# Kernel tuning notes

Measured on AMD Instinct MI355X. Metric: run time of the kernel, lower is better.

The kernel has to match this reference:

```python
import jax, jax.numpy as jnp
import numpy as np

N_NODES = 100000
N_EDGES = 1600000
D_FEAT = 64


def setup_inputs() -> dict:
    key = jax.random.key(0)
    k1, k2, k3, k4 = jax.random.split(key, 4)
    input = jax.random.normal(k1, (N_NODES, D_FEAT), dtype=jnp.float32)
    edge_weight = jax.random.uniform(k2, (N_EDGES,), dtype=jnp.float32)
    edge_src = jax.random.randint(k3, (N_EDGES,), 0, N_NODES, dtype=jnp.int64)
    edge_dst = jax.random.randint(k4, (N_EDGES,), 0, N_NODES, dtype=jnp.int64)
    return {"input": input, "edge_weight": edge_weight,
            "edge_src": edge_src, "edge_dst": edge_dst}


def reference(input, edge_weight, edge_src, edge_dst):
    # message: gather source node features, scale by edge weight -> (|E|, d)
    message = input[edge_src] * edge_weight[:, None]
    # aggregate: scatter-add edge messages to destination nodes -> (|V|, d)
    update = jax.ops.segment_sum(message, edge_dst, num_segments=input.shape[0])
    # combine: residual combination of input and update
    return input + update
```

## Files before the change

kernel.cpp:

```cpp
#include <hip/hip_runtime.h>
#include <hip/hip_bf16.h>

#define D_FEAT 64
#define NPB 64
#define NPB_SHIFT 6
#define NL1 128
#define L1_T 512
#define MAX_NB 2048
#define SCAN_T 256
#define SCAN_PER_T 8
#define SCAN_CHUNK (SCAN_T * SCAN_PER_T)
#define SRC_BITS 17
#define SRC_MASK 0x1FFFF
#define CVT_BLOCKS 1024
#define W_SCALE 32768.0f
#define W_INV (1.0f / 32768.0f)
#define SG_T 256
#define MAX_REC 4096

typedef unsigned int uint_t;

__device__ inline unsigned short f32_to_bf16_rn(float f) {
    uint_t x = __float_as_uint(f);
    uint_t r = (x + 0x7fffu + ((x >> 16) & 1u)) >> 16;
    return (unsigned short)r;
}

__global__ void __launch_bounds__(L1_T)
mp_pre_kernel(const int* __restrict__ edst,
              int* __restrict__ counts_T,
              int n_edges, int nb_buckets,
              int* __restrict__ pub) {
    __shared__ int hist[MAX_NB];
    int t = threadIdx.x;
    int b = blockIdx.x;
    if (b == 0)
        for (int i = t; i < 256; i += L1_T) pub[i] = 0;
    for (int k = t; k < nb_buckets; k += L1_T) hist[k] = 0;
    __syncthreads();
    int epb = (n_edges + NL1 - 1) / NL1;
    int lo = b * epb;
    int hi = min(n_edges, lo + epb);
    for (int i = lo + t; i < hi; i += L1_T)
        atomicAdd(&hist[edst[i] >> NPB_SHIFT], 1);
    __syncthreads();
    for (int k = t; k < nb_buckets; k += L1_T)
        counts_T[k * NL1 + b + 1] = hist[k];
    if (b == 0 && t == 0) counts_T[0] = 0;
}

__global__ void mp_scanP_kernel(int* __restrict__ a, int n,
                                int* __restrict__ pub) {
    __shared__ int tsum[SCAN_T];
    __shared__ int red[SCAN_T];
    int t = threadIdx.x, bid = blockIdx.x;
    int base = bid * SCAN_CHUNK + t * SCAN_PER_T;
    int v[SCAN_PER_T];
    int s = 0;
    #pragma unroll
    for (int j = 0; j < SCAN_PER_T; ++j) {
        int idx = base + j;
        v[j] = (idx < n) ? a[idx] : 0;
        s += v[j];
    }
    tsum[t] = s;
    __syncthreads();
    #pragma unroll
    for (int off = 1; off < SCAN_T; off <<= 1) {
        int u = (t >= off) ? tsum[t - off] : 0;
        __syncthreads();
        tsum[t] += u;
        __syncthreads();
    }
    if (t == SCAN_T - 1) atomicExch(&pub[bid], tsum[t] + 1);
    int ls = 0;
    for (int i = t; i < bid; i += SCAN_T) {
        int p;
        while ((p = atomicAdd(&pub[i], 0)) == 0) {}
        ls += p - 1;
    }
    red[t] = ls;
    __syncthreads();
    #pragma unroll
    for (int off = 128; off > 0; off >>= 1) {
        if (t < off) red[t] += red[t + off];
        __syncthreads();
    }
    int run = red[0] + ((t == 0) ? 0 : tsum[t - 1]);
    #pragma unroll
    for (int j = 0; j < SCAN_PER_T; ++j) {
        int idx = base + j;
        run += v[j];
        if (idx < n) a[idx] = run;
    }
}

__global__ void __launch_bounds__(L1_T)
mp_l1scatter_kernel(const int* __restrict__ esrc,
                    const int* __restrict__ edst,
                    const float* __restrict__ ew,
                    const int* __restrict__ counts_T,
                    int2* __restrict__ elistA,
                    int n_edges, int nb_buckets,
                    const float2* __restrict__ in2,
                    uint_t* __restrict__ bfrow, int ncvt) {
    __shared__ int cur[MAX_NB];
    int t = threadIdx.x;
    int b = blockIdx.x;
    if (b < NL1) {
        for (int k = t; k < nb_buckets; k += L1_T)
            cur[k] = counts_T[k * NL1 + b];
        __syncthreads();
        int epb = (n_edges + NL1 - 1) / NL1;
        int lo = b * epb;
        int hi = min(n_edges, lo + epb);
        for (int i = lo + t; i < hi; i += L1_T) {
            int d = edst[i];
            int pos = atomicAdd(&cur[d >> NPB_SHIFT], 1);
            elistA[pos] = make_int2(esrc[i] | ((d & (NPB - 1)) << SRC_BITS),
                                    __float_as_int(ew[i]));
        }
    } else {
        int g0 = (b - NL1) * L1_T + t;
        int stride = CVT_BLOCKS * L1_T;
        for (int g = g0; g < ncvt; g += stride) {
            float2 v = in2[g];
            bfrow[g] = (uint_t)f32_to_bf16_rn(v.x) |
                       ((uint_t)f32_to_bf16_rn(v.y) << 16);
        }
    }
}

__global__ void __launch_bounds__(SG_T)
mp_sortgather_kernel(const float* __restrict__ input,
                     const uint_t* __restrict__ bfrow,
                     const int2* __restrict__ elistA,
                     const int* __restrict__ counts_T,
                     float* __restrict__ out,
                     int n_nodes, int n_edges, int nb_buckets) {
    __shared__ int nh[NPB];
    __shared__ int cur[NPB];
    __shared__ uint_t rec[MAX_REC];
    int k = blockIdx.x;
    int t = threadIdx.x;
    int base = counts_T[k * NL1];
    int end  = (k + 1 < nb_buckets) ? counts_T[(k + 1) * NL1] : n_edges;
    int cnt  = end - base;

    int wv = t >> 6;
    int lane = t & 63;
    int h = lane >> 5, l5 = lane & 31;

    if (cnt <= MAX_REC) {
        if (t < NPB) nh[t] = 0;
        __syncthreads();
        for (int i = t; i < cnt; i += SG_T)
            atomicAdd(&nh[(elistA[base + i].x >> SRC_BITS) & (NPB - 1)], 1);
        __syncthreads();
        #pragma unroll
        for (int off = 1; off < NPB; off <<= 1) {
            int v = (t < NPB && t >= off) ? nh[t - off] : 0;
            __syncthreads();
            if (t < NPB) nh[t] += v;
            __syncthreads();
        }
        if (t < NPB) cur[t] = (t == 0) ? 0 : nh[t - 1];
        __syncthreads();
        for (int i = t; i < cnt; i += SG_T) {
            int2 r = elistA[base + i];
            int node = (r.x >> SRC_BITS) & (NPB - 1);
            int pos = atomicAdd(&cur[node], 1);
            int w15 = (int)(__int_as_float(r.y) * W_SCALE + 0.5f);
            w15 = min(32767, max(0, w15));
            rec[pos] = (uint_t)(r.x & SRC_MASK) | ((uint_t)w15 << 17);
        }
        __syncthreads();

        for (int node = wv; node < NPB; node += (SG_T / 64)) {
            int g = k * NPB + node;
            if (g >= n_nodes) break;
            int sb = (node == 0) ? 0 : nh[node - 1];
            int cn = nh[node] - sb;
            float ax = 0.0f, ay = 0.0f;
            int j = 0;
            for (; j + 16 <= cn; j += 16) {
                uint_t rr[8], u[8];
                #pragma unroll
                for (int q = 0; q < 8; ++q) rr[q] = rec[sb + j + 2 * q + h];
                #pragma unroll
                for (int q = 0; q < 8; ++q)
                    u[q] = bfrow[((rr[q] & SRC_MASK) << 5) + l5];
                #pragma unroll
                for (int q = 0; q < 8; ++q) {
                    float w = (float)(rr[q] >> 17) * W_INV;
                    ax = fmaf(__uint_as_float(u[q] << 16), w, ax);
                    ay = fmaf(__uint_as_float(u[q] & 0xffff0000u), w, ay);
                }
            }
            for (; j < cn; j += 2) {
                int jj = j + h;
                if (jj < cn) {
                    uint_t rr = rec[sb + jj];
                    uint_t u = bfrow[((rr & SRC_MASK) << 5) + l5];
                    float w = (float)(rr >> 17) * W_INV;
                    ax = fmaf(__uint_as_float(u << 16), w, ax);
                    ay = fmaf(__uint_as_float(u & 0xffff0000u), w, ay);
                }
            }
            ax += __shfl_xor(ax, 32, 64);
            ay += __shfl_xor(ay, 32, 64);
            if (h == 0) {
                float2 inp = ((const float2*)input)[((long long)g << 5) + l5];
                float2 o;
                o.x = inp.x + ax;
                o.y = inp.y + ay;
                ((float2*)out)[((long long)g << 5) + l5] = o;
            }
        }
    } else {
        for (int node = wv; node < NPB; node += (SG_T / 64)) {
            int g = k * NPB + node;
            if (g >= n_nodes) break;
            float ax = 0.0f, ay = 0.0f;
            for (int i = h; i < cnt; i += 2) {
                int2 r = elistA[base + i];
                if (((r.x >> SRC_BITS) & (NPB - 1)) == node) {
                    uint_t u = bfrow[(((uint_t)r.x & SRC_MASK) << 5) + l5];
                    float w = __int_as_float(r.y);
                    ax = fmaf(__uint_as_float(u << 16), w, ax);
                    ay = fmaf(__uint_as_float(u & 0xffff0000u), w, ay);
                }
            }
            ax += __shfl_xor(ax, 32, 64);
            ay += __shfl_xor(ay, 32, 64);
            if (h == 0) {
                float2 inp = ((const float2*)input)[((long long)g << 5) + l5];
                float2 o;
                o.x = inp.x + ax;
                o.y = inp.y + ay;
                ((float2*)out)[((long long)g << 5) + l5] = o;
            }
        }
    }
}

__global__ void mp_copy_kernel(const float4* __restrict__ in,
                               float4* __restrict__ out, int n4) {
    int i = blockIdx.x * blockDim.x + threadIdx.x;
    if (i < n4) out[i] = in[i];
}

__global__ void mp_scatter_kernel(const float* __restrict__ input,
                                  const float* __restrict__ ew,
                                  const int* __restrict__ esrc,
                                  const int* __restrict__ edst,
                                  float* __restrict__ out, int n_edges) {
    int tid = blockIdx.x * blockDim.x + threadIdx.x;
    int e = tid >> 6;
    if (e >= n_edges) return;
    int lane = tid & 63;
    float v = input[(long long)esrc[e] * D_FEAT + lane] * ew[e];
    atomicAdd(&out[(long long)edst[e] * D_FEAT + lane], v);
}

extern "C" void kernel_launch(void* const* d_in, const int* in_sizes, int n_in,
                              void* d_out, int out_size, void* d_ws, size_t ws_size,
                              hipStream_t stream) {
    const float* input = (const float*)d_in[0];
    const float* ew    = (const float*)d_in[1];
    const int* esrc    = (const int*)d_in[2];
    const int* edst    = (const int*)d_in[3];
    float* out = (float*)d_out;

    int n_nodes = in_sizes[0] / D_FEAT;
    int n_edges = in_sizes[1];

    int nb_buckets = (n_nodes + NPB - 1) / NPB;
    int n_scan = nb_buckets * NL1 + 1;
    int nbs = (n_scan + SCAN_CHUNK - 1) / SCAN_CHUNK;

    size_t head_ints = (size_t)n_scan + 256;
    size_t elist_off = (head_ints * 4 + 255) & ~(size_t)255;
    size_t elistA_bytes = (size_t)n_edges * 8;
    size_t bf_bytes = (size_t)n_nodes * (D_FEAT * 2);
    size_t needed = elist_off + elistA_bytes + bf_bytes;

    bool ok = (ws_size >= needed) && (nb_buckets <= MAX_NB) &&
              (n_nodes <= (1 << SRC_BITS)) && (nbs <= 256);

    if (ok) {
        int* counts_T = (int*)d_ws;
        int* pub      = counts_T + n_scan;
        int2* elistA  = (int2*)((char*)d_ws + elist_off);
        uint_t* bfrow = (uint_t*)((char*)d_ws + elist_off + elistA_bytes);
        int ncvt = n_nodes * (D_FEAT / 2);

        mp_pre_kernel<<<NL1, L1_T, 0, stream>>>(
            edst, counts_T, n_edges, nb_buckets, pub);
        mp_scanP_kernel<<<nbs, SCAN_T, 0, stream>>>(counts_T, n_scan, pub);
        mp_l1scatter_kernel<<<NL1 + CVT_BLOCKS, L1_T, 0, stream>>>(
            esrc, edst, ew, counts_T, elistA, n_edges, nb_buckets,
            (const float2*)input, bfrow, ncvt);
        mp_sortgather_kernel<<<nb_buckets, SG_T, 0, stream>>>(
            input, bfrow, elistA, counts_T, out, n_nodes, n_edges, nb_buckets);
    } else {
        int n4 = (n_nodes * D_FEAT) / 4;
        mp_copy_kernel<<<(n4 + 255) / 256, 256, 0, stream>>>(
            (const float4*)input, (float4*)out, n4);
        long long total = (long long)n_edges * 64;
        mp_scatter_kernel<<<(int)((total + 255) / 256), 256, 0, stream>>>(
            input, ew, esrc, edst, out, n_edges);
    }
}
```

Before: 105.6 us.

## Replace per-block transposed count scan with global bucket histogram and atomic scatter

Drops the per-block transposed count matrix, whose scan covered about 200k entries. In its place a global per-bucket histogram is built with atomics, scanned by a single 1024-thread block, and edges are scattered with global atomic cursors. The bf16 conversion moves into the histogram kernel instead of the scatter kernel. This shrinks the scan work and the decoupled-lookback sync, at the cost of a memset launch, heavy global atomic contention on about 1563 bucket cursors in the scatter, and a nondeterministic edge order within each bucket.

```diff
diff --git a/kernel.cpp b/kernel.cpp
--- a/kernel.cpp
+++ b/kernel.cpp
@@ -4,15 +4,12 @@
 #define D_FEAT 64
 #define NPB 64
 #define NPB_SHIFT 6
-#define NL1 128
-#define L1_T 512
+#define HB 128
+#define HB_T 512
+#define CVT_BLOCKS 1024
 #define MAX_NB 2048
-#define SCAN_T 256
-#define SCAN_PER_T 8
-#define SCAN_CHUNK (SCAN_T * SCAN_PER_T)
 #define SRC_BITS 17
 #define SRC_MASK 0x1FFFF
-#define CVT_BLOCKS 1024
 #define W_SCALE 32768.0f
 #define W_INV (1.0f / 32768.0f)
 #define SG_T 256
@@ -26,103 +23,29 @@
     return (unsigned short)r;
 }
 
-__global__ void __launch_bounds__(L1_T)
-mp_pre_kernel(const int* __restrict__ edst,
-              int* __restrict__ counts_T,
-              int n_edges, int nb_buckets,
-              int* __restrict__ pub) {
+__global__ void __launch_bounds__(HB_T)
+mp_histcvt_kernel(const int* __restrict__ edst,
+                  int* __restrict__ cnt_g,
+                  int n_edges, int nb_buckets,
+                  const float2* __restrict__ in2,
+                  uint_t* __restrict__ bfrow, int ncvt) {
     __shared__ int hist[MAX_NB];
     int t = threadIdx.x;
     int b = blockIdx.x;
-    if (b == 0)
-        for (int i = t; i < 256; i += L1_T) pub[i] = 0;
-    for (int k = t; k < nb_buckets; k += L1_T) hist[k] = 0;
-    __syncthreads();
-    int epb = (n_edges + NL1 - 1) / NL1;
-    int lo = b * epb;
-    int hi = min(n_edges, lo + epb);
-    for (int i = lo + t; i < hi; i += L1_T)
-        atomicAdd(&hist[edst[i] >> NPB_SHIFT], 1);
-    __syncthreads();
-    for (int k = t; k < nb_buckets; k += L1_T)
-        counts_T[k * NL1 + b + 1] = hist[k];
-    if (b == 0 && t == 0) counts_T[0] = 0;
-}
-
-__global__ void mp_scanP_kernel(int* __restrict__ a, int n,
-                                int* __restrict__ pub) {
-    __shared__ int tsum[SCAN_T];
-    __shared__ int red[SCAN_T];
-    int t = threadIdx.x, bid = blockIdx.x;
-    int base = bid * SCAN_CHUNK + t * SCAN_PER_T;
-    int v[SCAN_PER_T];
-    int s = 0;
-    #pragma unroll
-    for (int j = 0; j < SCAN_PER_T; ++j) {
-        int idx = base + j;
-        v[j] = (idx < n) ? a[idx] : 0;
-        s += v[j];
-    }
-    tsum[t] = s;
-    __syncthreads();
-    #pragma unroll
-    for (int off = 1; off < SCAN_T; off <<= 1) {
-        int u = (t >= off) ? tsum[t - off] : 0;
-        __syncthreads();
-        tsum[t] += u;
-        __syncthreads();
-    }
-    if (t == SCAN_T - 1) atomicExch(&pub[bid], tsum[t] + 1);
-    int ls = 0;
-    for (int i = t; i < bid; i += SCAN_T) {
-        int p;
-        while ((p = atomicAdd(&pub[i], 0)) == 0) {}
-        ls += p - 1;
-    }
-    red[t] = ls;
-    __syncthreads();
-    #pragma unroll
-    for (int off = 128; off > 0; off >>= 1) {
-        if (t < off) red[t] += red[t + off];
-        __syncthreads();
-    }
-    int run = red[0] + ((t == 0) ? 0 : tsum[t - 1]);
-    #pragma unroll
-    for (int j = 0; j < SCAN_PER_T; ++j) {
-        int idx = base + j;
-        run += v[j];
-        if (idx < n) a[idx] = run;
-    }
-}
-
-__global__ void __launch_bounds__(L1_T)
-mp_l1scatter_kernel(const int* __restrict__ esrc,
-                    const int* __restrict__ edst,
-                    const float* __restrict__ ew,
-                    const int* __restrict__ counts_T,
-                    int2* __restrict__ elistA,
-                    int n_edges, int nb_buckets,
-                    const float2* __restrict__ in2,
-                    uint_t* __restrict__ bfrow, int ncvt) {
-    __shared__ int cur[MAX_NB];
-    int t = threadIdx.x;
-    int b = blockIdx.x;
-    if (b < NL1) {
-        for (int k = t; k < nb_buckets; k += L1_T)
-            cur[k] = counts_T[k * NL1 + b];
-        __syncthreads();
-        int epb = (n_edges + NL1 - 1) / NL1;
+    if (b < HB) {
+        for (int k = t; k < nb_buckets; k += HB_T) hist[k] = 0;
+        __syncthreads();
+        int epb = (n_edges + HB - 1) / HB;
         int lo = b * epb;
         int hi = min(n_edges, lo + epb);
-        for (int i = lo + t; i < hi; i += L1_T) {
-            int d = edst[i];
-            int pos = atomicAdd(&cur[d >> NPB_SHIFT], 1);
-            elistA[pos] = make_int2(esrc[i] | ((d & (NPB - 1)) << SRC_BITS),
-                                    __float_as_int(ew[i]));
-        }
+        for (int i = lo + t; i < hi; i += HB_T)
+            atomicAdd(&hist[edst[i] >> NPB_SHIFT], 1);
+        __syncthreads();
+        for (int k = t; k < nb_buckets; k += HB_T)
+            if (hist[k] != 0) atomicAdd(&cnt_g[k], hist[k]);
     } else {
-        int g0 = (b - NL1) * L1_T + t;
-        int stride = CVT_BLOCKS * L1_T;
+        int g0 = (b - HB) * HB_T + t;
+        int stride = CVT_BLOCKS * HB_T;
         for (int g = g0; g < ncvt; g += stride) {
             float2 v = in2[g];
             bfrow[g] = (uint_t)f32_to_bf16_rn(v.x) |
@@ -131,11 +54,50 @@
     }
 }
 
+__global__ void __launch_bounds__(1024)
+mp_tinyscan_kernel(const int* __restrict__ cnt_g,
+                   int* __restrict__ start, int* __restrict__ cur,
+                   int nb_buckets) {
+    __shared__ int ts[1024];
+    int t = threadIdx.x;
+    int i0 = 2 * t, i1 = 2 * t + 1;
+    int a0 = (i0 < nb_buckets) ? cnt_g[i0] : 0;
+    int a1 = (i1 < nb_buckets) ? cnt_g[i1] : 0;
+    ts[t] = a0 + a1;
+    __syncthreads();
+    #pragma unroll
+    for (int off = 1; off < 1024; off <<= 1) {
+        int u = (t >= off) ? ts[t - off] : 0;
+        __syncthreads();
+        ts[t] += u;
+        __syncthreads();
+    }
+    int p = (t == 0) ? 0 : ts[t - 1];
+    if (i0 < nb_buckets) { start[i0] = p;      cur[i0] = p; }
+    if (i1 < nb_buckets) { start[i1] = p + a0; cur[i1] = p + a0; }
+    if (t == 0) start[nb_buckets] = ts[1023];
+}
+
+__global__ void mp_ascatter_kernel(const int* __restrict__ esrc,
+                                   const int* __restrict__ edst,
+                                   const float* __restrict__ ew,
+                                   int* __restrict__ cur,
+                                   int2* __restrict__ elistA, int n_edges) {
+    int tid = blockIdx.x * blockDim.x + threadIdx.x;
+    int stride = gridDim.x * blockDim.x;
+    for (int i = tid; i < n_edges; i += stride) {
+        int d = edst[i];
+        int pos = atomicAdd(&cur[d >> NPB_SHIFT], 1);
+        elistA[pos] = make_int2(esrc[i] | ((d & (NPB - 1)) << SRC_BITS),
+                                __float_as_int(ew[i]));
+    }
+}
+
 __global__ void __launch_bounds__(SG_T)
 mp_sortgather_kernel(const float* __restrict__ input,
                      const uint_t* __restrict__ bfrow,
                      const int2* __restrict__ elistA,
-                     const int* __restrict__ counts_T,
+                     const int* __restrict__ start,
                      float* __restrict__ out,
                      int n_nodes, int n_edges, int nb_buckets) {
     __shared__ int nh[NPB];
@@ -143,8 +105,8 @@
     __shared__ uint_t rec[MAX_REC];
     int k = blockIdx.x;
     int t = threadIdx.x;
-    int base = counts_T[k * NL1];
-    int end  = (k + 1 < nb_buckets) ? counts_T[(k + 1) * NL1] : n_edges;
+    int base = start[k];
+    int end  = start[k + 1];
     int cnt  = end - base;
 
     int wv = t >> 6;
@@ -276,33 +238,32 @@
     int n_edges = in_sizes[1];
 
     int nb_buckets = (n_nodes + NPB - 1) / NPB;
-    int n_scan = nb_buckets * NL1 + 1;
-    int nbs = (n_scan + SCAN_CHUNK - 1) / SCAN_CHUNK;
-
-    size_t head_ints = (size_t)n_scan + 256;
+
+    size_t head_ints = (size_t)nb_buckets * 3 + 1;
     size_t elist_off = (head_ints * 4 + 255) & ~(size_t)255;
     size_t elistA_bytes = (size_t)n_edges * 8;
     size_t bf_bytes = (size_t)n_nodes * (D_FEAT * 2);
     size_t needed = elist_off + elistA_bytes + bf_bytes;
 
     bool ok = (ws_size >= needed) && (nb_buckets <= MAX_NB) &&
-              (n_nodes <= (1 << SRC_BITS)) && (nbs <= 256);
+              (n_nodes <= (1 << SRC_BITS));
 
     if (ok) {
-        int* counts_T = (int*)d_ws;
-        int* pub      = counts_T + n_scan;
+        int* cnt_g  = (int*)d_ws;
+        int* start  = cnt_g + nb_buckets;
+        int* cur    = start + nb_buckets + 1;
         int2* elistA  = (int2*)((char*)d_ws + elist_off);
         uint_t* bfrow = (uint_t*)((char*)d_ws + elist_off + elistA_bytes);
         int ncvt = n_nodes * (D_FEAT / 2);
 
-        mp_pre_kernel<<<NL1, L1_T, 0, stream>>>(
-            edst, counts_T, n_edges, nb_buckets, pub);
-        mp_scanP_kernel<<<nbs, SCAN_T, 0, stream>>>(counts_T, n_scan, pub);
-        mp_l1scatter_kernel<<<NL1 + CVT_BLOCKS, L1_T, 0, stream>>>(
-            esrc, edst, ew, counts_T, elistA, n_edges, nb_buckets,
-            (const float2*)input, bfrow, ncvt);
+        hipMemsetAsync(cnt_g, 0, nb_buckets * sizeof(int), stream);
+        mp_histcvt_kernel<<<HB + CVT_BLOCKS, HB_T, 0, stream>>>(
+            edst, cnt_g, n_edges, nb_buckets, (const float2*)input, bfrow, ncvt);
+        mp_tinyscan_kernel<<<1, 1024, 0, stream>>>(cnt_g, start, cur, nb_buckets);
+        mp_ascatter_kernel<<<2048, 256, 0, stream>>>(esrc, edst, ew, cur,
+                                                     elistA, n_edges);
         mp_sortgather_kernel<<<nb_buckets, SG_T, 0, stream>>>(
-            input, bfrow, elistA, counts_T, out, n_nodes, n_edges, nb_buckets);
+            input, bfrow, elistA, start, out, n_nodes, n_edges, nb_buckets);
     } else {
         int n4 = (n_nodes * D_FEAT) / 4;
         mp_copy_kernel<<<(n4 + 255) / 256, 256, 0, stream>>>(
```

After: 321.5 us. 3.04x slower.
